# Kernel tuning notes

Measured on AMD Instinct MI355X. Metric: run time of the kernel, lower is better.

## Reference

```python
import jax, jax.numpy as jnp
import numpy as np

BSZ, NLVL, E, H, FFN = 8, 4, 512, 8, 2048
D = E // H
NNZ = 131072
LMAX = NNZ // BSZ  # equal per-batch counts -> static padded length
THETA = 10.0


def _layernorm(x, g, b):
    mu = x.mean(-1, keepdims=True)
    var = ((x - mu) ** 2).mean(-1, keepdims=True)
    return (x - mu) / jnp.sqrt(var + 1e-5) * g + b


def _rope(x, pos, freqs):
    # x: [N, E], pos: [N] float, freqs: [H, D/2] -> rotate interleaved pairs per head
    N = x.shape[0]
    nh, half = freqs.shape
    xr = x.reshape(N, nh, half, 2)
    ang = pos[:, None, None] * freqs[None]            # [N, H, D/2]
    c, s = jnp.cos(ang), jnp.sin(ang)
    x1, x2 = xr[..., 0], xr[..., 1]
    out = jnp.stack([x1 * c - x2 * s, x1 * s + x2 * c], axis=-1)
    return out.reshape(N, -1)


def setup_inputs() -> dict:
    key = jax.random.key(0)
    ks = jax.random.split(key, 8)
    bg = jax.random.normal(ks[0], (BSZ, NLVL, E), jnp.float32)
    feature_values = jax.random.normal(ks[1], (NNZ, E), jnp.float32)
    # coalesced sparse COO -> batch indices sorted; equal counts per batch for static shapes
    feature_batch_idx = (jnp.arange(NNZ, dtype=jnp.int32) // LMAX)
    feature_level_idx = jax.random.randint(ks[2], (NNZ,), 0, NLVL, dtype=jnp.int32)
    s = 1.0 / np.sqrt(E)
    Wq = jax.random.normal(ks[3], (E, E), jnp.float32) * s
    Wkv = jax.random.normal(ks[4], (E, 2 * E), jnp.float32) * s
    Wo = jax.random.normal(ks[5], (E, E), jnp.float32) * s
    freqs = THETA ** (-jnp.arange(D // 2, dtype=jnp.float32) * 2.0 / D)
    rope_freqs = jnp.tile(freqs[None, :], (H, 1))  # share_heads=False: per-head table
    ln_attn_g, ln_attn_b = jnp.ones(E, jnp.float32), jnp.zeros(E, jnp.float32)
    ln_ffn_g, ln_ffn_b = jnp.ones(E, jnp.float32), jnp.zeros(E, jnp.float32)
    W1 = jax.random.normal(ks[6], (E, FFN), jnp.float32) * s
    b1 = jnp.zeros(FFN, jnp.float32)
    W2 = jax.random.normal(ks[7], (FFN, E), jnp.float32) * (1.0 / np.sqrt(FFN))
    b2 = jnp.zeros(E, jnp.float32)
    return {
        'bg': bg, 'feature_values': feature_values,
        'feature_batch_idx': feature_batch_idx, 'feature_level_idx': feature_level_idx,
        'Wq': Wq, 'Wkv': Wkv, 'Wo': Wo, 'rope_freqs': rope_freqs,
        'ln_attn_g': ln_attn_g, 'ln_attn_b': ln_attn_b,
        'ln_ffn_g': ln_ffn_g, 'ln_ffn_b': ln_ffn_b,
        'W1': W1, 'b1': b1, 'W2': W2, 'b2': b2,
        'max_len': LMAX,
    }


def reference(bg, feature_values, feature_batch_idx, feature_level_idx,
              Wq, Wkv, Wo, rope_freqs, ln_attn_g, ln_attn_b,
              ln_ffn_g, ln_ffn_b, W1, b1, W2, b2, max_len):
    bsz, nlvl, e = bg.shape
    nh = rope_freqs.shape[0]
    d = e // nh
    nnz = feature_values.shape[0]

    # --- attention block (pre-norm) ---
    residual = bg
    x = _layernorm(bg, ln_attn_g, ln_attn_b)
    q = (x @ Wq).reshape(bsz * nlvl, e)
    kv = feature_values @ Wkv
    k, v = kv[:, :e], kv[:, e:]

    # RoPE on level indices (replicates original's repeat_interleave ordering: level = i // bsz)
    q_lvl = (jnp.arange(bsz * nlvl) // bsz).astype(jnp.float32)
    q = _rope(q, q_lvl, rope_freqs)
    k = _rope(k, feature_level_idx.astype(jnp.float32), rope_freqs)

    # concatenated (ragged) -> padded per batch
    counts = jax.ops.segment_sum(jnp.ones(nnz, jnp.int32), feature_batch_idx, num_segments=bsz)
    offsets = jnp.concatenate([jnp.zeros(1, jnp.int32), jnp.cumsum(counts)[:-1].astype(jnp.int32)])
    pos = jnp.arange(nnz, dtype=jnp.int32) - offsets[feature_batch_idx]
    k_pad = jnp.zeros((bsz, max_len, e), k.dtype).at[feature_batch_idx, pos].set(k)
    v_pad = jnp.zeros((bsz, max_len, e), v.dtype).at[feature_batch_idx, pos].set(v)
    pad_mask = jnp.arange(max_len)[None, :] >= counts[:, None]  # True at padding

    # SDPA
    qh = q.reshape(bsz, nlvl, nh, d).transpose(0, 2, 1, 3)
    kh = k_pad.reshape(bsz, max_len, nh, d).transpose(0, 2, 1, 3)
    vh = v_pad.reshape(bsz, max_len, nh, d).transpose(0, 2, 1, 3)
    scores = jnp.einsum('bhqd,bhkd->bhqk', qh, kh) / jnp.sqrt(jnp.asarray(d, qh.dtype))
    scores = jnp.where(pad_mask[:, None, None, :], -jnp.inf, scores)
    attn = jax.nn.softmax(scores, axis=-1)
    o = jnp.einsum('bhqk,bhkd->bhqd', attn, vh).transpose(0, 2, 1, 3).reshape(bsz, nlvl, e)
    o = o @ Wo + residual

    # --- FFN block (pre-norm) ---
    y = _layernorm(o, ln_ffn_g, ln_ffn_b)
    y = jax.nn.relu(y @ W1 + b1) @ W2 + b2
    return o + y
```

## Files before the change

kernel.cpp:

```cpp
#include <hip/hip_runtime.h>
#include <hip/hip_bf16.h>
#include <math.h>

#define BSZ 8
#define NLVL 4
#define E 512
#define H 8
#define D 64
#define FFN 2048
#define NNZ 131072
#define NQ 32
#define P32 32
#define NEGF -3.0e38f

typedef __attribute__((ext_vector_type(8))) short bf16x8;
typedef __attribute__((ext_vector_type(4))) float f32x4;

#define WS_QROT   16
#define WS_WSUM   (WS_QROT + NQ*E)
#define WS_OATT   (WS_WSUM + BSZ*P32*E)
#define WS_O2     (WS_OATT + NQ*E)
#define WS_Y      (WS_O2 + NQ*E)
#define WS_HID    (WS_Y + NQ*E)
#define WS_PART   (WS_HID + NQ*FFN)
#define WS_ML     (WS_PART + 512*P32*E)
#define WS_WALL   (WS_ML + 512*P32*2)

__device__ inline short f2bf(float x) {
    __hip_bfloat16 h = __float2bfloat16(x);
    union { __hip_bfloat16 v; short s; } u; u.v = h; return u.s;
}

__global__ void k_zero(int* wsi) {
    if (blockIdx.x == 0 && threadIdx.x < 8) wsi[threadIdx.x] = 0;
}

__global__ void k_hist(const int* __restrict__ fb, int* wsi) {
    __shared__ int h[8];
    int t = threadIdx.x;
    if (t < 8) h[t] = 0;
    __syncthreads();
    for (int j = blockIdx.x * 256 + t; j < NNZ; j += gridDim.x * 256)
        atomicAdd(&h[fb[j]], 1);
    __syncthreads();
    if (t < 8) atomicAdd(&wsi[t], h[t]);
}

__global__ void k_off(int* wsi) {
    if (threadIdx.x == 0) {
        int run = 0;
        for (int b = 0; b < 8; b++) { wsi[8 + b] = run; run += wsi[b]; }
    }
}

__global__ void k_qrot(const float* __restrict__ bg, const float* __restrict__ Wq,
                       const float* __restrict__ rf, const float* __restrict__ g,
                       const float* __restrict__ bb, float* __restrict__ ws) {
    __shared__ float xr[E];
    __shared__ float qrow[E];
    __shared__ float red[8];
    int r = blockIdx.x, t = threadIdx.x;
    float v0 = bg[r * E + t], v1 = bg[r * E + t + 256];
    float s = v0 + v1;
    for (int o = 32; o > 0; o >>= 1) s += __shfl_down(s, o, 64);
    if ((t & 63) == 0) red[t >> 6] = s;
    __syncthreads();
    if (t == 0) red[0] = (red[0] + red[1] + red[2] + red[3]) * (1.0f / E);
    __syncthreads();
    float mu = red[0];
    __syncthreads();
    float d0 = v0 - mu, d1 = v1 - mu;
    s = d0 * d0 + d1 * d1;
    for (int o = 32; o > 0; o >>= 1) s += __shfl_down(s, o, 64);
    if ((t & 63) == 0) red[t >> 6] = s;
    __syncthreads();
    if (t == 0) red[0] = rsqrtf((red[0] + red[1] + red[2] + red[3]) * (1.0f / E) + 1e-5f);
    __syncthreads();
    float rstd = red[0];
    xr[t] = d0 * rstd * g[t] + bb[t];
    xr[t + 256] = d1 * rstd * g[t + 256] + bb[t + 256];
    __syncthreads();
    for (int half = 0; half < 2; half++) {
        int c = t + half * 256;
        float acc = 0.f;
        for (int e = 0; e < E; e++) acc += xr[e] * Wq[e * E + c];
        qrow[c] = acc;
    }
    __syncthreads();
    int c0 = 2 * t, c1 = c0 + 1;
    int h = c0 >> 6, ii = (c0 & 63) >> 1;
    float freq = rf[h * 32 + ii];
    float pos = (float)(r >> 3);
    float a = pos * freq, ca = cosf(a), sa = sinf(a);
    float x1 = qrow[c0], x2 = qrow[c1];
    float* qr = ws + WS_QROT + r * E;
    qr[c0] = x1 * ca - x2 * sa;
    qr[c1] = x1 * sa + x2 * ca;
}

__global__ void k_wtil(const float* __restrict__ Wkv, const float* __restrict__ rf,
                       const float* __restrict__ ws, short* __restrict__ wall) {
    __shared__ float u[D];
    int blk = blockIdx.x;
    int h = blk & 7, lvl = (blk >> 3) & 3, r = blk >> 5;
    int b = r >> 2, l = r & 3;
    int t = threadIdx.x;
    const float* qr = ws + WS_QROT + r * E + h * D;
    if (t < 32) {
        float freq = rf[h * 32 + t];
        float a = (float)lvl * freq;
        float ca = cosf(a), sa = sinf(a);
        float x1 = qr[2 * t], x2 = qr[2 * t + 1];
        u[2 * t] = x1 * ca + x2 * sa;
        u[2 * t + 1] = -x1 * sa + x2 * ca;
    }
    __syncthreads();
    int n = lvl * 32 + l * 8 + h;
    short* wrow_out = wall + ((size_t)(b * 128 + n)) * E;
    for (int rep = 0; rep < 8; rep++) {
        int e = t + rep * 64;
        const float* wrow = Wkv + (size_t)e * (2 * E) + h * D;
        float acc = 0.f;
#pragma unroll
        for (int c = 0; c < D; c++) acc += wrow[c] * u[c];
        wrow_out[e] = f2bf(acc * 0.125f);
    }
}

#define KSTR 520
#define TSTR 40
__global__ __launch_bounds__(256, 2) void k_flash(
    const float* __restrict__ fv, const int* __restrict__ fl,
    const short* __restrict__ wall, const int* __restrict__ wsi,
    const int* __restrict__ maxlen, float* __restrict__ part, float* __restrict__ ml) {
    __shared__ short kbuf[32 * KSTR];
    __shared__ short fvT[512 * TSTR];
    __shared__ short pbuf[32 * TSTR];
    __shared__ float mbuf[4 * 32];
    __shared__ float lpart[4 * 32];
    __shared__ float alph[32];
    __shared__ float mrun[32];
    __shared__ float lrun[32];

    int t = threadIdx.x;
    int w = t >> 6, lane = t & 63, col = lane & 15, quad = lane >> 4;
    int b = blockIdx.x, kc = blockIdx.y;
    int cnt = wsi[b], mlen = maxlen[0];
    int lim = cnt < mlen ? cnt : mlen;
    int off = wsi[8 + b];
    int kbase = kc * 256;
    int nv = lim - kbase; if (nv > 256) nv = 256; if (nv < 0) nv = 0;

    if (t < 32) { mrun[t] = NEGF; lrun[t] = 0.f; }

    f32x4 acc_o[2][8];
#pragma unroll
    for (int mt = 0; mt < 2; mt++)
#pragma unroll
        for (int nt = 0; nt < 8; nt++) acc_o[mt][nt] = f32x4{0.f, 0.f, 0.f, 0.f};

    const short* wallb = wall + (size_t)b * 128 * E;
    int sj = (t & 15) * 2;
    int se = (t >> 4) * 32;

    for (int s = 0; s < 8; s++) {
        int vs = nv - s * 32;
        if (vs <= 0) break;
        __syncthreads();
        {
            int g0 = off + kbase + s * 32 + sj;
            int g1 = g0 + 1;
            if (g0 > NNZ - 1) g0 = NNZ - 1;
            if (g1 > NNZ - 1) g1 = NNZ - 1;
            const float* r0 = fv + (size_t)g0 * E + se;
            const float* r1 = fv + (size_t)g1 * E + se;
#pragma unroll
            for (int i = 0; i < 8; i++) {
                float4 x0 = *(const float4*)(r0 + i * 4);
                float4 x1 = *(const float4*)(r1 + i * 4);
                int e = se + i * 4;
                *(__hip_bfloat162*)&kbuf[sj * KSTR + e]       = __float22bfloat162_rn(float2{x0.x, x0.y});
                *(__hip_bfloat162*)&kbuf[sj * KSTR + e + 2]   = __float22bfloat162_rn(float2{x0.z, x0.w});
                *(__hip_bfloat162*)&kbuf[(sj+1) * KSTR + e]   = __float22bfloat162_rn(float2{x1.x, x1.y});
                *(__hip_bfloat162*)&kbuf[(sj+1) * KSTR + e+2] = __float22bfloat162_rn(float2{x1.z, x1.w});
                *(__hip_bfloat162*)&fvT[(e + 0) * TSTR + sj] = __float22bfloat162_rn(float2{x0.x, x1.x});
                *(__hip_bfloat162*)&fvT[(e + 1) * TSTR + sj] = __float22bfloat162_rn(float2{x0.y, x1.y});
                *(__hip_bfloat162*)&fvT[(e + 2) * TSTR + sj] = __float22bfloat162_rn(float2{x0.z, x1.z});
                *(__hip_bfloat162*)&fvT[(e + 3) * TSTR + sj] = __float22bfloat162_rn(float2{x0.w, x1.w});
            }
        }
        __syncthreads();
        f32x4 acc_s[2][2];
#pragma unroll
        for (int mt = 0; mt < 2; mt++)
#pragma unroll
            for (int kt = 0; kt < 2; kt++) acc_s[mt][kt] = f32x4{0.f, 0.f, 0.f, 0.f};
        {
            const short* wr0 = wallb + (size_t)(w * 32 + col) * E + quad * 8;
            const short* wr1 = wr0 + (size_t)16 * E;
            const short* kb0 = &kbuf[col * KSTR + quad * 8];
            const short* kb1 = &kbuf[(16 + col) * KSTR + quad * 8];
#pragma unroll
            for (int ks = 0; ks < 16; ks++) {
                int e0 = ks * 32;
                bf16x8 A0 = *(const bf16x8*)(wr0 + e0);
                bf16x8 A1 = *(const bf16x8*)(wr1 + e0);
                bf16x8 B0 = *(const bf16x8*)(kb0 + e0);
                bf16x8 B1 = *(const bf16x8*)(kb1 + e0);
                acc_s[0][0] = __builtin_amdgcn_mfma_f32_16x16x32_bf16(A0, B0, acc_s[0][0], 0, 0, 0);
                acc_s[0][1] = __builtin_amdgcn_mfma_f32_16x16x32_bf16(A0, B1, acc_s[0][1], 0, 0, 0);
                acc_s[1][0] = __builtin_amdgcn_mfma_f32_16x16x32_bf16(A1, B0, acc_s[1][0], 0, 0, 0);
                acc_s[1][1] = __builtin_amdgcn_mfma_f32_16x16x32_bf16(A1, B1, acc_s[1][1], 0, 0, 0);
            }
        }
        int kg0 = off + kbase + s * 32 + col;
        int kg1 = kg0 + 16;
        if (kg0 > NNZ - 1) kg0 = NNZ - 1;
        if (kg1 > NNZ - 1) kg1 = NNZ - 1;
        int lv0 = fl[kg0], lv1 = fl[kg1];
        bool valid0 = (s * 32 + col) < nv;
        bool valid1 = (s * 32 + 16 + col) < nv;
        bool sel0 = valid0 && (lv0 == w);
        bool sel1 = valid1 && (lv1 == w);
#pragma unroll
        for (int mt = 0; mt < 2; mt++) {
#pragma unroll
            for (int r = 0; r < 4; r++) {
                float v0 = sel0 ? acc_s[mt][0][r] : NEGF;
                float v1 = sel1 ? acc_s[mt][1][r] : NEGF;
                float v = fmaxf(v0, v1);
#pragma unroll
                for (int msk = 1; msk < 16; msk <<= 1) v = fmaxf(v, __shfl_xor(v, msk, 16));
                if (col == 0) mbuf[w * 32 + mt * 16 + quad * 4 + r] = v;
            }
        }
        __syncthreads();
        if (t < 32) {
            int p = t;
            float mo = mrun[p];
            float mn = mo;
            mn = fmaxf(mn, mbuf[p]);
            mn = fmaxf(mn, mbuf[32 + p]);
            mn = fmaxf(mn, mbuf[64 + p]);
            mn = fmaxf(mn, mbuf[96 + p]);
            alph[p] = expf(mo - mn);
            mrun[p] = mn;
        }
        __syncthreads();
        float mr[2][4], ar[2][4];
#pragma unroll
        for (int mt = 0; mt < 2; mt++)
#pragma unroll
            for (int r = 0; r < 4; r++) {
                int p = mt * 16 + quad * 4 + r;
                mr[mt][r] = mrun[p];
                ar[mt][r] = alph[p];
            }
#pragma unroll
        for (int mt = 0; mt < 2; mt++) {
#pragma unroll
            for (int r = 0; r < 4; r++) {
                int p = mt * 16 + quad * 4 + r;
                float ls = 0.f;
                {
                    if (sel0) {
                        float pv = expf(acc_s[mt][0][r] - mr[mt][r]);
                        pbuf[p * TSTR + col] = f2bf(pv);
                        ls += pv;
                    } else if (w == 0 && !valid0) {
                        pbuf[p * TSTR + col] = 0;
                    }
                    if (sel1) {
                        float pv = expf(acc_s[mt][1][r] - mr[mt][r]);
                        pbuf[p * TSTR + 16 + col] = f2bf(pv);
                        ls += pv;
                    } else if (w == 0 && !valid1) {
                        pbuf[p * TSTR + 16 + col] = 0;
                    }
                }
#pragma unroll
                for (int msk = 1; msk < 16; msk <<= 1) ls += __shfl_xor(ls, msk, 16);
                if (col == 0) lpart[w * 32 + p] = ls;
            }
        }
#pragma unroll
        for (int mt = 0; mt < 2; mt++)
#pragma unroll
            for (int nt = 0; nt < 8; nt++)
#pragma unroll
                for (int r = 0; r < 4; r++) acc_o[mt][nt][r] *= ar[mt][r];
        __syncthreads();
        {
            bf16x8 Ap0 = *(const bf16x8*)&pbuf[col * TSTR + quad * 8];
            bf16x8 Ap1 = *(const bf16x8*)&pbuf[(16 + col) * TSTR + quad * 8];
            const short* bt = &fvT[(size_t)(w * 128 + col) * TSTR + quad * 8];
#pragma unroll
            for (int nt = 0; nt < 8; nt++) {
                bf16x8 Bf = *(const bf16x8*)(bt + (size_t)nt * 16 * TSTR);
                acc_o[0][nt] = __builtin_amdgcn_mfma_f32_16x16x32_bf16(Ap0, Bf, acc_o[0][nt], 0, 0, 0);
                acc_o[1][nt] = __builtin_amdgcn_mfma_f32_16x16x32_bf16(Ap1, Bf, acc_o[1][nt], 0, 0, 0);
            }
        }
        if (t < 32) {
            int p = t;
            lrun[p] = lrun[p] * alph[p] + (lpart[p] + lpart[32 + p] + lpart[64 + p] + lpart[96 + p]);
        }
    }
    size_t pbase = ((size_t)(b * 64 + kc) * P32) * E;
#pragma unroll
    for (int mt = 0; mt < 2; mt++)
#pragma unroll
        for (int r = 0; r < 4; r++) {
            int p = mt * 16 + quad * 4 + r;
#pragma unroll
            for (int nt = 0; nt < 8; nt++) {
                int e = w * 128 + nt * 16 + col;
                part[pbase + (size_t)p * E + e] = acc_o[mt][nt][r];
            }
        }
    if (t < 32) {
        size_t idx = (size_t)(b * 64 + kc) * P32 + t;
        ml[idx * 2] = mrun[t];
        ml[idx * 2 + 1] = lrun[t];
    }
}

__global__ void k_merge(const float* __restrict__ part, const float* __restrict__ ml,
                        float* __restrict__ wsum) {
    __shared__ float wexp[64];
    int b = blockIdx.x >> 5, p = blockIdx.x & 31;
    int t = threadIdx.x;
    float M = NEGF;
    for (int kc = 0; kc < 64; kc++)
        M = fmaxf(M, ml[((size_t)(b * 64 + kc) * P32 + p) * 2]);
    float denom = 0.f;
    for (int kc = 0; kc < 64; kc++) {
        size_t idx = ((size_t)(b * 64 + kc) * P32 + p) * 2;
        denom += ml[idx + 1] * expf(ml[idx] - M);
    }
    if (t < 64)
        wexp[t] = expf(ml[((size_t)(b * 64 + t) * P32 + p) * 2] - M);
    __syncthreads();
    float inv = 1.0f / denom;
    for (int half = 0; half < 2; half++) {
        int e = t + half * 256;
        float acc = 0.f;
        for (int kc = 0; kc < 64; kc++)
            acc += part[((size_t)(b * 64 + kc) * P32 + p) * E + e] * wexp[kc];
        wsum[((size_t)(b * P32 + p)) * E + e] = acc * inv;
    }
}

__global__ void k_oproj(const float* __restrict__ wsum, const float* __restrict__ Wkv,
                        float* __restrict__ oatt) {
    __shared__ float Aw[NQ][E];
    int h = blockIdx.x >> 2, ct = blockIdx.x & 3;
    int t = threadIdx.x;
    {
        int rr = t >> 3, x = (t & 7) * 64;
        int row = (rr >> 2) * P32 + (rr & 3) * 8 + h;
#pragma unroll
        for (int q4 = 0; q4 < 16; q4++)
            *(float4*)&Aw[rr][x + q4 * 4] = *(const float4*)&wsum[(size_t)row * E + x + q4 * 4];
    }
    __syncthreads();
#pragma unroll
    for (int rep = 0; rep < 2; rep++) {
        int idx = rep * 256 + t;
        int rr = idx >> 4, cl = idx & 15;
        int c = h * D + ct * 16 + cl;
        float acc = 0.f;
        for (int e = 0; e < E; e++) acc += Aw[rr][e] * Wkv[(size_t)e * (2 * E) + E + c];
        oatt[rr * E + c] = acc;
    }
}

__global__ void k_wo(const float* __restrict__ oatt, const float* __restrict__ Wo,
                     const float* __restrict__ bg, float* __restrict__ o2) {
    __shared__ float Aw[NQ * E];
    int t = threadIdx.x;
#pragma unroll
    for (int q = 0; q < 16; q++) {
        int i = (q * 256 + t) * 4;
        *(float4*)&Aw[i] = *(const float4*)&oatt[i];
    }
    __syncthreads();
    int ct = blockIdx.x;
#pragma unroll
    for (int rep = 0; rep < 4; rep++) {
        int idx = rep * 256 + t;
        int rr = idx >> 5, cl = idx & 31;
        int c = ct * 32 + cl;
        float acc = bg[rr * E + c];
        for (int e = 0; e < E; e++) acc += Aw[rr * E + e] * Wo[(size_t)e * E + c];
        o2[rr * E + c] = acc;
    }
}

__global__ void k_ln2(const float* __restrict__ o2, const float* __restrict__ g,
                      const float* __restrict__ bb, float* __restrict__ y) {
    __shared__ float red[8];
    int r = blockIdx.x, t = threadIdx.x;
    float v0 = o2[r * E + t], v1 = o2[r * E + t + 256];
    float s = v0 + v1;
    for (int o = 32; o > 0; o >>= 1) s += __shfl_down(s, o, 64);
    if ((t & 63) == 0) red[t >> 6] = s;
    __syncthreads();
    if (t == 0) red[0] = (red[0] + red[1] + red[2] + red[3]) * (1.0f / E);
    __syncthreads();
    float mu = red[0];
    __syncthreads();
    float d0 = v0 - mu, d1 = v1 - mu;
    s = d0 * d0 + d1 * d1;
    for (int o = 32; o > 0; o >>= 1) s += __shfl_down(s, o, 64);
    if ((t & 63) == 0) red[t >> 6] = s;
    __syncthreads();
    if (t == 0) red[0] = rsqrtf((red[0] + red[1] + red[2] + red[3]) * (1.0f / E) + 1e-5f);
    __syncthreads();
    float rstd = red[0];
    y[r * E + t] = d0 * rstd * g[t] + bb[t];
    y[r * E + t + 256] = d1 * rstd * g[t + 256] + bb[t + 256];
}

__global__ void k_ffn1(const float* __restrict__ y, const float* __restrict__ W1,
                       const float* __restrict__ b1, float* __restrict__ hid) {
    __shared__ float Aw[NQ * E];
    int t = threadIdx.x;
#pragma unroll
    for (int q = 0; q < 16; q++) {
        int i = (q * 256 + t) * 4;
        *(float4*)&Aw[i] = *(const float4*)&y[i];
    }
    __syncthreads();
    int ft = blockIdx.x;
#pragma unroll
    for (int rep = 0; rep < 4; rep++) {
        int idx = rep * 256 + t;
        int rr = idx >> 5, fl = idx & 31;
        int f = ft * 32 + fl;
        float acc = b1[f];
        for (int e = 0; e < E; e++) acc += Aw[rr * E + e] * W1[(size_t)e * FFN + f];
        hid[rr * FFN + f] = fmaxf(acc, 0.f);
    }
}

__global__ void k_ffn2(const float* __restrict__ hid, const float* __restrict__ W2,
                       const float* __restrict__ b2, const float* __restrict__ o2,
                       float* __restrict__ out) {
    int ct = blockIdx.x;
    int t = threadIdx.x;
#pragma unroll
    for (int rep = 0; rep < 2; rep++) {
        int idx = rep * 256 + t;
        int rr = idx >> 4, cl = idx & 15;
        int c = ct * 16 + cl;
        float acc = b2[c] + o2[rr * E + c];
        for (int f = 0; f < FFN; f++) acc += hid[rr * FFN + f] * W2[(size_t)f * E + c];
        out[rr * E + c] = acc;
    }
}

extern "C" void kernel_launch(void* const* d_in, const int* in_sizes, int n_in,
                              void* d_out, int out_size, void* d_ws, size_t ws_size,
                              hipStream_t stream) {
    const float* bg  = (const float*)d_in[0];
    const float* fv  = (const float*)d_in[1];
    const int*   fb  = (const int*)d_in[2];
    const int*   fl  = (const int*)d_in[3];
    const float* Wq  = (const float*)d_in[4];
    const float* Wkv = (const float*)d_in[5];
    const float* Wo  = (const float*)d_in[6];
    const float* rf  = (const float*)d_in[7];
    const float* lag = (const float*)d_in[8];
    const float* lab = (const float*)d_in[9];
    const float* lfg = (const float*)d_in[10];
    const float* lfb = (const float*)d_in[11];
    const float* W1  = (const float*)d_in[12];
    const float* b1  = (const float*)d_in[13];
    const float* W2  = (const float*)d_in[14];
    const float* b2  = (const float*)d_in[15];
    const int* maxlen = (const int*)d_in[16];
    float* ws = (float*)d_ws;
    int* wsi = (int*)d_ws;
    short* wall = (short*)(ws + WS_WALL);
    float* out = (float*)d_out;

    hipLaunchKernelGGL(k_zero, dim3(1), dim3(64), 0, stream, wsi);
    hipLaunchKernelGGL(k_hist, dim3(128), dim3(256), 0, stream, fb, wsi);
    hipLaunchKernelGGL(k_off, dim3(1), dim3(64), 0, stream, wsi);
    hipLaunchKernelGGL(k_qrot, dim3(NQ), dim3(256), 0, stream, bg, Wq, rf, lag, lab, ws);
    hipLaunchKernelGGL(k_wtil, dim3(NQ * NLVL * H), dim3(64), 0, stream, Wkv, rf, ws, wall);
    hipLaunchKernelGGL(k_flash, dim3(BSZ, 64), dim3(256), 0, stream,
                       fv, fl, wall, wsi, maxlen, ws + WS_PART, ws + WS_ML);
    hipLaunchKernelGGL(k_merge, dim3(BSZ * P32), dim3(256), 0, stream,
                       ws + WS_PART, ws + WS_ML, ws + WS_WSUM);
    hipLaunchKernelGGL(k_oproj, dim3(H * 4), dim3(256), 0, stream,
                       ws + WS_WSUM, Wkv, ws + WS_OATT);
    hipLaunchKernelGGL(k_wo, dim3(16), dim3(256), 0, stream,
                       ws + WS_OATT, Wo, bg, ws + WS_O2);
    hipLaunchKernelGGL(k_ln2, dim3(NQ), dim3(256), 0, stream,
                       ws + WS_O2, lfg, lfb, ws + WS_Y);
    hipLaunchKernelGGL(k_ffn1, dim3(FFN / 32), dim3(256), 0, stream,
                       ws + WS_Y, W1, b1, ws + WS_HID);
    hipLaunchKernelGGL(k_ffn2, dim3(E / 16), dim3(256), 0, stream,
                       ws + WS_HID, W2, b2, ws + WS_O2, out);
}
```

Before: 864.8 us.

## Fuse prologue and epilogue kernels into persistent grid-barrier kernels with split-K atomics

Merges the histogram/offset kernels with a Wkv transpose into one launch, fuses the q projection, RoPE and W-tilde construction into one kernel reading a transposed Wkv for coalesced access, and collapses merge, output projection, Wo, layernorm and both FFN GEMMs into a single 256-block kernel. Stages are separated by software grid barriers, and the GEMMs use split-K with atomicAdd. The goal is to cut launch overhead and spread the small epilogue GEMMs across many more blocks. The risks are deadlock if not all 256 blocks are co-resident, nondeterministic float atomics, and barrier spin cost.

```diff
diff --git a/kernel.cpp b/kernel.cpp
--- a/kernel.cpp
+++ b/kernel.cpp
@@ -31,33 +31,80 @@
     union { __hip_bfloat16 v; short s; } u; u.v = h; return u.s;
 }
 
-__global__ void k_zero(int* wsi) {
-    if (blockIdx.x == 0 && threadIdx.x < 8) wsi[threadIdx.x] = 0;
-}
-
-__global__ void k_hist(const int* __restrict__ fb, int* wsi) {
-    __shared__ int h[8];
+__global__ __launch_bounds__(1024) void k_pretr(const float* __restrict__ Wkv,
+                                                float* __restrict__ wkt,
+                                                const int* __restrict__ fb,
+                                                int* __restrict__ wsi) {
+    __shared__ float tile[64][65];
     int t = threadIdx.x;
-    if (t < 8) h[t] = 0;
-    __syncthreads();
-    for (int j = blockIdx.x * 256 + t; j < NNZ; j += gridDim.x * 256)
-        atomicAdd(&h[fb[j]], 1);
-    __syncthreads();
-    if (t < 8) atomicAdd(&wsi[t], h[t]);
-}
-
-__global__ void k_off(int* wsi) {
-    if (threadIdx.x == 0) {
+    if (blockIdx.x < 64) {
+        if (t < 256) {
+            int ct = blockIdx.x & 7, et = blockIdx.x >> 3;
+            int tc = t & 63, tr = t >> 6;
+#pragma unroll
+            for (int i = 0; i < 16; i++) {
+                int e = et * 64 + tr + i * 4;
+                tile[tr + i * 4][tc] = Wkv[(size_t)e * (2 * E) + ct * 64 + tc];
+            }
+        }
+        __syncthreads();
+        if (t < 256) {
+            int ct = blockIdx.x & 7, et = blockIdx.x >> 3;
+            int tc = t & 63, tr = t >> 6;
+#pragma unroll
+            for (int i = 0; i < 16; i++) {
+                int c = tr + i * 4;
+                wkt[(size_t)(ct * 64 + c) * E + et * 64 + tc] = tile[tc][c];
+            }
+        }
+        return;
+    }
+    int c[8];
+#pragma unroll
+    for (int q = 0; q < 8; q++) c[q] = 0;
+    for (int j = t; j < NNZ; j += 1024) {
+        int v = fb[j];
+#pragma unroll
+        for (int q = 0; q < 8; q++) c[q] += (v == q) ? 1 : 0;
+    }
+#pragma unroll
+    for (int q = 0; q < 8; q++)
+        for (int o = 32; o > 0; o >>= 1) c[q] += __shfl_down(c[q], o, 64);
+    __shared__ int hs[16][8];
+    int w = t >> 6;
+    if ((t & 63) == 0) {
+#pragma unroll
+        for (int q = 0; q < 8; q++) hs[w][q] = c[q];
+    }
+    __syncthreads();
+    if (t == 0) {
+        int tot[8];
+#pragma unroll
+        for (int q = 0; q < 8; q++) {
+            int s = 0;
+            for (int ww = 0; ww < 16; ww++) s += hs[ww][q];
+            tot[q] = s;
+        }
         int run = 0;
-        for (int b = 0; b < 8; b++) { wsi[8 + b] = run; run += wsi[b]; }
-    }
-}
-
-__global__ void k_qrot(const float* __restrict__ bg, const float* __restrict__ Wq,
-                       const float* __restrict__ rf, const float* __restrict__ g,
-                       const float* __restrict__ bb, float* __restrict__ ws) {
+        for (int b = 0; b < 8; b++) {
+            wsi[b] = tot[b];
+            wsi[8 + b] = run;
+            run += tot[b];
+        }
+    }
+}
+
+__global__ __launch_bounds__(256) void k_qw(const float* __restrict__ bg,
+                                            const float* __restrict__ Wq,
+                                            const float* __restrict__ wkt,
+                                            const float* __restrict__ rf,
+                                            const float* __restrict__ g,
+                                            const float* __restrict__ bb,
+                                            short* __restrict__ wall) {
     __shared__ float xr[E];
     __shared__ float qrow[E];
+    __shared__ float qrot[E];
+    __shared__ float ubuf[32 * 64];
     __shared__ float red[8];
     int r = blockIdx.x, t = threadIdx.x;
     float v0 = bg[r * E + t], v1 = bg[r * E + t + 256];
@@ -81,49 +128,51 @@
     xr[t + 256] = d1 * rstd * g[t + 256] + bb[t + 256];
     __syncthreads();
     for (int half = 0; half < 2; half++) {
-        int c = t + half * 256;
+        int cc = t + half * 256;
         float acc = 0.f;
-        for (int e = 0; e < E; e++) acc += xr[e] * Wq[e * E + c];
-        qrow[c] = acc;
-    }
-    __syncthreads();
-    int c0 = 2 * t, c1 = c0 + 1;
-    int h = c0 >> 6, ii = (c0 & 63) >> 1;
-    float freq = rf[h * 32 + ii];
-    float pos = (float)(r >> 3);
-    float a = pos * freq, ca = cosf(a), sa = sinf(a);
-    float x1 = qrow[c0], x2 = qrow[c1];
-    float* qr = ws + WS_QROT + r * E;
-    qr[c0] = x1 * ca - x2 * sa;
-    qr[c1] = x1 * sa + x2 * ca;
-}
-
-__global__ void k_wtil(const float* __restrict__ Wkv, const float* __restrict__ rf,
-                       const float* __restrict__ ws, short* __restrict__ wall) {
-    __shared__ float u[D];
-    int blk = blockIdx.x;
-    int h = blk & 7, lvl = (blk >> 3) & 3, r = blk >> 5;
-    int b = r >> 2, l = r & 3;
-    int t = threadIdx.x;
-    const float* qr = ws + WS_QROT + r * E + h * D;
-    if (t < 32) {
-        float freq = rf[h * 32 + t];
+        for (int e = 0; e < E; e++) acc += xr[e] * Wq[e * E + cc];
+        qrow[cc] = acc;
+    }
+    __syncthreads();
+    {
+        int c0 = 2 * t, c1 = c0 + 1;
+        int h = c0 >> 6, ii = (c0 & 63) >> 1;
+        float freq = rf[h * 32 + ii];
+        float pos = (float)(r >> 3);
+        float a = pos * freq, ca = cosf(a), sa = sinf(a);
+        float x1 = qrow[c0], x2 = qrow[c1];
+        qrot[c0] = x1 * ca - x2 * sa;
+        qrot[c1] = x1 * sa + x2 * ca;
+    }
+    __syncthreads();
+#pragma unroll
+    for (int i = 0; i < 4; i++) {
+        int tk = i * 256 + t;
+        int combo = tk >> 5, pr = tk & 31;
+        int h = combo >> 2, lvl = combo & 3;
+        float freq = rf[h * 32 + pr];
         float a = (float)lvl * freq;
         float ca = cosf(a), sa = sinf(a);
-        float x1 = qr[2 * t], x2 = qr[2 * t + 1];
-        u[2 * t] = x1 * ca + x2 * sa;
-        u[2 * t + 1] = -x1 * sa + x2 * ca;
-    }
-    __syncthreads();
-    int n = lvl * 32 + l * 8 + h;
-    short* wrow_out = wall + ((size_t)(b * 128 + n)) * E;
-    for (int rep = 0; rep < 8; rep++) {
-        int e = t + rep * 64;
-        const float* wrow = Wkv + (size_t)e * (2 * E) + h * D;
-        float acc = 0.f;
-#pragma unroll
-        for (int c = 0; c < D; c++) acc += wrow[c] * u[c];
-        wrow_out[e] = f2bf(acc * 0.125f);
+        float x1 = qrot[h * D + 2 * pr], x2 = qrot[h * D + 2 * pr + 1];
+        ubuf[combo * 64 + 2 * pr] = x1 * ca + x2 * sa;
+        ubuf[combo * 64 + 2 * pr + 1] = -x1 * sa + x2 * ca;
+    }
+    __syncthreads();
+    int b = r >> 2, l = r & 3;
+    for (int combo = 0; combo < 32; combo++) {
+        int h = combo >> 2, lvl = combo & 3;
+        const float* wt = wkt + (size_t)(h * D) * E;
+        float acc0 = 0.f, acc1 = 0.f;
+#pragma unroll
+        for (int c = 0; c < D; c++) {
+            float uc = ubuf[combo * 64 + c];
+            acc0 += wt[(size_t)c * E + t] * uc;
+            acc1 += wt[(size_t)c * E + t + 256] * uc;
+        }
+        int n = lvl * 32 + l * 8 + h;
+        short* o = wall + ((size_t)(b * 128 + n)) * E;
+        o[t] = f2bf(acc0 * 0.125f);
+        o[t + 256] = f2bf(acc1 * 0.125f);
     }
 }
 
@@ -132,7 +181,8 @@
 __global__ __launch_bounds__(256, 2) void k_flash(
     const float* __restrict__ fv, const int* __restrict__ fl,
     const short* __restrict__ wall, const int* __restrict__ wsi,
-    const int* __restrict__ maxlen, float* __restrict__ part, float* __restrict__ ml) {
+    const int* __restrict__ maxlen, float* __restrict__ part, float* __restrict__ ml,
+    int* __restrict__ gcnt) {
     __shared__ short kbuf[32 * KSTR];
     __shared__ short fvT[512 * TSTR];
     __shared__ short pbuf[32 * TSTR];
@@ -145,6 +195,7 @@
     int t = threadIdx.x;
     int w = t >> 6, lane = t & 63, col = lane & 15, quad = lane >> 4;
     int b = blockIdx.x, kc = blockIdx.y;
+    if (b == 0 && kc == 0 && t == 0) *gcnt = 0;
     int cnt = wsi[b], mlen = maxlen[0];
     int lim = cnt < mlen ? cnt : mlen;
     int off = wsi[8 + b];
@@ -325,138 +376,186 @@
     }
 }
 
-__global__ void k_merge(const float* __restrict__ part, const float* __restrict__ ml,
-                        float* __restrict__ wsum) {
-    __shared__ float wexp[64];
-    int b = blockIdx.x >> 5, p = blockIdx.x & 31;
-    int t = threadIdx.x;
-    float M = NEGF;
-    for (int kc = 0; kc < 64; kc++)
-        M = fmaxf(M, ml[((size_t)(b * 64 + kc) * P32 + p) * 2]);
-    float denom = 0.f;
-    for (int kc = 0; kc < 64; kc++) {
-        size_t idx = ((size_t)(b * 64 + kc) * P32 + p) * 2;
-        denom += ml[idx + 1] * expf(ml[idx] - M);
-    }
-    if (t < 64)
-        wexp[t] = expf(ml[((size_t)(b * 64 + t) * P32 + p) * 2] - M);
-    __syncthreads();
-    float inv = 1.0f / denom;
-    for (int half = 0; half < 2; half++) {
-        int e = t + half * 256;
-        float acc = 0.f;
+__device__ inline void gridbar(int* cnt, int target) {
+    __syncthreads();
+    __threadfence();
+    if (threadIdx.x == 0) {
+        atomicAdd(cnt, 1);
+        while (atomicAdd(cnt, 0) < target)
+            __builtin_amdgcn_s_sleep(8);
+    }
+    __syncthreads();
+    __threadfence();
+}
+
+__global__ __launch_bounds__(256) void k_epi(
+    const float* __restrict__ part, const float* __restrict__ ml,
+    float* __restrict__ wsum, float* __restrict__ oatt, float* __restrict__ o2,
+    float* __restrict__ y, float* __restrict__ hid,
+    const float* __restrict__ Wkv, const float* __restrict__ Wo,
+    const float* __restrict__ bg, const float* __restrict__ lfg, const float* __restrict__ lfb,
+    const float* __restrict__ W1, const float* __restrict__ b1,
+    const float* __restrict__ W2, const float* __restrict__ b2,
+    float* __restrict__ out, int* __restrict__ gcnt) {
+    __shared__ float smem[32 * 128];
+    int bid = blockIdx.x, t = threadIdx.x;
+
+    {
+        if (t < 64) oatt[bid * 64 + t] = 0.f;
+        int b = bid & 7, p = bid >> 3;
+        float M = NEGF;
         for (int kc = 0; kc < 64; kc++)
-            acc += part[((size_t)(b * 64 + kc) * P32 + p) * E + e] * wexp[kc];
-        wsum[((size_t)(b * P32 + p)) * E + e] = acc * inv;
-    }
-}
-
-__global__ void k_oproj(const float* __restrict__ wsum, const float* __restrict__ Wkv,
-                        float* __restrict__ oatt) {
-    __shared__ float Aw[NQ][E];
-    int h = blockIdx.x >> 2, ct = blockIdx.x & 3;
-    int t = threadIdx.x;
+            M = fmaxf(M, ml[((size_t)(b * 64 + kc) * P32 + p) * 2]);
+        float denom = 0.f;
+        for (int kc = 0; kc < 64; kc++) {
+            size_t idx = ((size_t)(b * 64 + kc) * P32 + p) * 2;
+            denom += ml[idx + 1] * expf(ml[idx] - M);
+        }
+        if (t < 64)
+            smem[t] = expf(ml[((size_t)(b * 64 + t) * P32 + p) * 2] - M);
+        __syncthreads();
+        float inv = 1.0f / denom;
+        for (int half = 0; half < 2; half++) {
+            int e = t + half * 256;
+            float acc = 0.f;
+            for (int kc = 0; kc < 64; kc++)
+                acc += part[((size_t)(b * 64 + kc) * P32 + p) * E + e] * smem[kc];
+            wsum[((size_t)(b * P32 + p)) * E + e] = acc * inv;
+        }
+    }
+    gridbar(gcnt, 256);
+
+    if (bid < 128) {
+        int ct = bid & 15, kc = bid >> 4;
+        int h = ct >> 1;
+        {
+            int rr = t >> 3, kk = (t & 7) * 8;
+            int wrow = (rr >> 2) * P32 + (rr & 3) * 8 + h;
+            const float* src = &wsum[(size_t)wrow * E + kc * 64 + kk];
+            *(float4*)&smem[rr * 64 + kk]     = *(const float4*)src;
+            *(float4*)&smem[rr * 64 + kk + 4] = *(const float4*)(src + 4);
+        }
+        __syncthreads();
+#pragma unroll
+        for (int rep = 0; rep < 4; rep++) {
+            int idx = rep * 256 + t;
+            int rr = idx >> 5, cl = idx & 31;
+            int c = ct * 32 + cl;
+            float acc = 0.f;
+            const float* wp = &Wkv[(size_t)(kc * 64) * (2 * E) + E + c];
+#pragma unroll
+            for (int k = 0; k < 64; k++) acc += smem[rr * 64 + k] * wp[(size_t)k * (2 * E)];
+            atomicAdd(&oatt[rr * E + c], acc);
+        }
+    } else {
+        if (t < 128) o2[(bid - 128) * 128 + t] = 0.f;
+    }
+    gridbar(gcnt, 512);
+
+    if (bid < 128) {
+        int ct = bid & 15, kc = bid >> 4;
+        {
+            int rr = t >> 3, kk = (t & 7) * 8;
+            const float* src = &oatt[(size_t)rr * E + kc * 64 + kk];
+            *(float4*)&smem[rr * 64 + kk]     = *(const float4*)src;
+            *(float4*)&smem[rr * 64 + kk + 4] = *(const float4*)(src + 4);
+        }
+        __syncthreads();
+#pragma unroll
+        for (int rep = 0; rep < 4; rep++) {
+            int idx = rep * 256 + t;
+            int rr = idx >> 5, cl = idx & 31;
+            int c = ct * 32 + cl;
+            float acc = (kc == 0) ? bg[rr * E + c] : 0.f;
+            const float* wp = &Wo[(size_t)(kc * 64) * E + c];
+#pragma unroll
+            for (int k = 0; k < 64; k++) acc += smem[rr * 64 + k] * wp[(size_t)k * E];
+            atomicAdd(&o2[rr * E + c], acc);
+        }
+    } else {
+        hid[(bid - 128) * 512 + t] = 0.f;
+        hid[(bid - 128) * 512 + 256 + t] = 0.f;
+    }
+    gridbar(gcnt, 768);
+
+    if (bid < 32) {
+        float* red = smem;
+        int r = bid;
+        float v0 = o2[r * E + t], v1 = o2[r * E + t + 256];
+        float s = v0 + v1;
+        for (int o = 32; o > 0; o >>= 1) s += __shfl_down(s, o, 64);
+        if ((t & 63) == 0) red[t >> 6] = s;
+        __syncthreads();
+        if (t == 0) red[0] = (red[0] + red[1] + red[2] + red[3]) * (1.0f / E);
+        __syncthreads();
+        float mu = red[0];
+        __syncthreads();
+        float d0 = v0 - mu, d1 = v1 - mu;
+        s = d0 * d0 + d1 * d1;
+        for (int o = 32; o > 0; o >>= 1) s += __shfl_down(s, o, 64);
+        if ((t & 63) == 0) red[t >> 6] = s;
+        __syncthreads();
+        if (t == 0) red[0] = rsqrtf((red[0] + red[1] + red[2] + red[3]) * (1.0f / E) + 1e-5f);
+        __syncthreads();
+        float rstd = red[0];
+        y[r * E + t] = d0 * rstd * lfg[t] + lfb[t];
+        y[r * E + t + 256] = d1 * rstd * lfg[t + 256] + lfb[t + 256];
+    } else if (bid < 160) {
+        if (t < 128) out[(bid - 32) * 128 + t] = 0.f;
+    }
+    gridbar(gcnt, 1024);
+
     {
-        int rr = t >> 3, x = (t & 7) * 64;
-        int row = (rr >> 2) * P32 + (rr & 3) * 8 + h;
-#pragma unroll
-        for (int q4 = 0; q4 < 16; q4++)
-            *(float4*)&Aw[rr][x + q4 * 4] = *(const float4*)&wsum[(size_t)row * E + x + q4 * 4];
-    }
-    __syncthreads();
-#pragma unroll
-    for (int rep = 0; rep < 2; rep++) {
-        int idx = rep * 256 + t;
-        int rr = idx >> 4, cl = idx & 15;
-        int c = h * D + ct * 16 + cl;
-        float acc = 0.f;
-        for (int e = 0; e < E; e++) acc += Aw[rr][e] * Wkv[(size_t)e * (2 * E) + E + c];
-        oatt[rr * E + c] = acc;
-    }
-}
-
-__global__ void k_wo(const float* __restrict__ oatt, const float* __restrict__ Wo,
-                     const float* __restrict__ bg, float* __restrict__ o2) {
-    __shared__ float Aw[NQ * E];
-    int t = threadIdx.x;
-#pragma unroll
-    for (int q = 0; q < 16; q++) {
-        int i = (q * 256 + t) * 4;
-        *(float4*)&Aw[i] = *(const float4*)&oatt[i];
-    }
-    __syncthreads();
-    int ct = blockIdx.x;
-#pragma unroll
-    for (int rep = 0; rep < 4; rep++) {
-        int idx = rep * 256 + t;
-        int rr = idx >> 5, cl = idx & 31;
-        int c = ct * 32 + cl;
-        float acc = bg[rr * E + c];
-        for (int e = 0; e < E; e++) acc += Aw[rr * E + e] * Wo[(size_t)e * E + c];
-        o2[rr * E + c] = acc;
-    }
-}
-
-__global__ void k_ln2(const float* __restrict__ o2, const float* __restrict__ g,
-                      const float* __restrict__ bb, float* __restrict__ y) {
-    __shared__ float red[8];
-    int r = blockIdx.x, t = threadIdx.x;
-    float v0 = o2[r * E + t], v1 = o2[r * E + t + 256];
-    float s = v0 + v1;
-    for (int o = 32; o > 0; o >>= 1) s += __shfl_down(s, o, 64);
-    if ((t & 63) == 0) red[t >> 6] = s;
-    __syncthreads();
-    if (t == 0) red[0] = (red[0] + red[1] + red[2] + red[3]) * (1.0f / E);
-    __syncthreads();
-    float mu = red[0];
-    __syncthreads();
-    float d0 = v0 - mu, d1 = v1 - mu;
-    s = d0 * d0 + d1 * d1;
-    for (int o = 32; o > 0; o >>= 1) s += __shfl_down(s, o, 64);
-    if ((t & 63) == 0) red[t >> 6] = s;
-    __syncthreads();
-    if (t == 0) red[0] = rsqrtf((red[0] + red[1] + red[2] + red[3]) * (1.0f / E) + 1e-5f);
-    __syncthreads();
-    float rstd = red[0];
-    y[r * E + t] = d0 * rstd * g[t] + bb[t];
-    y[r * E + t + 256] = d1 * rstd * g[t + 256] + bb[t + 256];
-}
-
-__global__ void k_ffn1(const float* __restrict__ y, const float* __restrict__ W1,
-                       const float* __restrict__ b1, float* __restrict__ hid) {
-    __shared__ float Aw[NQ * E];
-    int t = threadIdx.x;
-#pragma unroll
-    for (int q = 0; q < 16; q++) {
-        int i = (q * 256 + t) * 4;
-        *(float4*)&Aw[i] = *(const float4*)&y[i];
-    }
-    __syncthreads();
-    int ft = blockIdx.x;
-#pragma unroll
-    for (int rep = 0; rep < 4; rep++) {
-        int idx = rep * 256 + t;
-        int rr = idx >> 5, fl = idx & 31;
-        int f = ft * 32 + fl;
-        float acc = b1[f];
-        for (int e = 0; e < E; e++) acc += Aw[rr * E + e] * W1[(size_t)e * FFN + f];
-        hid[rr * FFN + f] = fmaxf(acc, 0.f);
-    }
-}
-
-__global__ void k_ffn2(const float* __restrict__ hid, const float* __restrict__ W2,
-                       const float* __restrict__ b2, const float* __restrict__ o2,
-                       float* __restrict__ out) {
-    int ct = blockIdx.x;
-    int t = threadIdx.x;
-#pragma unroll
-    for (int rep = 0; rep < 2; rep++) {
-        int idx = rep * 256 + t;
-        int rr = idx >> 4, cl = idx & 15;
-        int c = ct * 16 + cl;
-        float acc = b2[c] + o2[rr * E + c];
-        for (int f = 0; f < FFN; f++) acc += hid[rr * FFN + f] * W2[(size_t)f * E + c];
-        out[rr * E + c] = acc;
+        int ft = bid & 63, kc = bid >> 6;
+        {
+            int rr = t >> 3, kk = (t & 7) * 16;
+            const float* src = &y[(size_t)rr * E + kc * 128 + kk];
+#pragma unroll
+            for (int j = 0; j < 4; j++)
+                *(float4*)&smem[rr * 128 + kk + j * 4] = *(const float4*)(src + j * 4);
+        }
+        __syncthreads();
+#pragma unroll
+        for (int rep = 0; rep < 4; rep++) {
+            int idx = rep * 256 + t;
+            int rr = idx >> 5, fc = idx & 31;
+            int f = ft * 32 + fc;
+            float acc = (kc == 0) ? b1[f] : 0.f;
+            const float* wp = &W1[(size_t)(kc * 128) * FFN + f];
+#pragma unroll
+            for (int k = 0; k < 128; k++) acc += smem[rr * 128 + k] * wp[(size_t)k * FFN];
+            atomicAdd(&hid[rr * FFN + f], acc);
+        }
+    }
+    gridbar(gcnt, 1280);
+
+    {
+        int ct = bid & 15, kc = bid >> 4;
+        __syncthreads();
+        {
+            int rr = t >> 3, kk = (t & 7) * 16;
+            const float* src = &hid[(size_t)rr * FFN + kc * 128 + kk];
+#pragma unroll
+            for (int j = 0; j < 4; j++) {
+                float4 v = *(const float4*)(src + j * 4);
+                smem[rr * 128 + kk + j * 4 + 0] = fmaxf(v.x, 0.f);
+                smem[rr * 128 + kk + j * 4 + 1] = fmaxf(v.y, 0.f);
+                smem[rr * 128 + kk + j * 4 + 2] = fmaxf(v.z, 0.f);
+                smem[rr * 128 + kk + j * 4 + 3] = fmaxf(v.w, 0.f);
+            }
+        }
+        __syncthreads();
+#pragma unroll
+        for (int rep = 0; rep < 4; rep++) {
+            int idx = rep * 256 + t;
+            int rr = idx >> 5, cl = idx & 31;
+            int c = ct * 32 + cl;
+            float acc = (kc == 0) ? (b2[c] + o2[rr * E + c]) : 0.f;
+            const float* wp = &W2[(size_t)(kc * 128) * E + c];
+#pragma unroll
+            for (int k = 0; k < 128; k++) acc += smem[rr * 128 + k] * wp[(size_t)k * E];
+            atomicAdd(&out[rr * E + c], acc);
+        }
     }
 }
 
@@ -483,25 +582,16 @@
     float* ws = (float*)d_ws;
     int* wsi = (int*)d_ws;
     short* wall = (short*)(ws + WS_WALL);
+    float* wkt = ws + WS_PART;
+    int* gcnt = (int*)(ws + WS_QROT);
     float* out = (float*)d_out;
 
-    hipLaunchKernelGGL(k_zero, dim3(1), dim3(64), 0, stream, wsi);
-    hipLaunchKernelGGL(k_hist, dim3(128), dim3(256), 0, stream, fb, wsi);
-    hipLaunchKernelGGL(k_off, dim3(1), dim3(64), 0, stream, wsi);
-    hipLaunchKernelGGL(k_qrot, dim3(NQ), dim3(256), 0, stream, bg, Wq, rf, lag, lab, ws);
-    hipLaunchKernelGGL(k_wtil, dim3(NQ * NLVL * H), dim3(64), 0, stream, Wkv, rf, ws, wall);
+    hipLaunchKernelGGL(k_pretr, dim3(65), dim3(1024), 0, stream, Wkv, wkt, fb, wsi);
+    hipLaunchKernelGGL(k_qw, dim3(NQ), dim3(256), 0, stream, bg, Wq, wkt, rf, lag, lab, wall);
     hipLaunchKernelGGL(k_flash, dim3(BSZ, 64), dim3(256), 0, stream,
-                       fv, fl, wall, wsi, maxlen, ws + WS_PART, ws + WS_ML);
-    hipLaunchKernelGGL(k_merge, dim3(BSZ * P32), dim3(256), 0, stream,
-                       ws + WS_PART, ws + WS_ML, ws + WS_WSUM);
-    hipLaunchKernelGGL(k_oproj, dim3(H * 4), dim3(256), 0, stream,
-                       ws + WS_WSUM, Wkv, ws + WS_OATT);
-    hipLaunchKernelGGL(k_wo, dim3(16), dim3(256), 0, stream,
-                       ws + WS_OATT, Wo, bg, ws + WS_O2);
-    hipLaunchKernelGGL(k_ln2, dim3(NQ), dim3(256), 0, stream,
-                       ws + WS_O2, lfg, lfb, ws + WS_Y);
-    hipLaunchKernelGGL(k_ffn1, dim3(FFN / 32), dim3(256), 0, stream,
-                       ws + WS_Y, W1, b1, ws + WS_HID);
-    hipLaunchKernelGGL(k_ffn2, dim3(E / 16), dim3(256), 0, stream,
-                       ws + WS_HID, W2, b2, ws + WS_O2, out);
-}
+                       fv, fl, wall, wsi, maxlen, ws + WS_PART, ws + WS_ML, gcnt);
+    hipLaunchKernelGGL(k_epi, dim3(256), dim3(256), 0, stream,
+                       ws + WS_PART, ws + WS_ML, ws + WS_WSUM, ws + WS_OATT, ws + WS_O2,
+                       ws + WS_Y, ws + WS_HID, Wkv, Wo, bg, lfg, lfb, W1, b1, W2, b2,
+                       out, gcnt);
+}
```

Result: slower. 938.3 us (+8.5%).
